# Optimization experiments

Measured on AMD Instinct MI355X. Metric: run time of the kernel, lower is better.

## Reference

```python
import jax, jax.numpy as jnp
import numpy as np

B, T, E, H, DK, FF = 8, 2048, 64, 8, 8, 256
EPS = 1e-5


def _ln(x, g, b):
    m = jnp.mean(x, axis=-1, keepdims=True)
    v = jnp.mean((x - m) ** 2, axis=-1, keepdims=True)
    return (x - m) * jax.lax.rsqrt(v + EPS) * g + b


def setup_inputs() -> dict:
    key = jax.random.key(0)
    ks = jax.random.split(key, 16)
    s = 0.05
    f32 = jnp.float32
    return {
        "x": jax.random.normal(ks[0], (B, T, E), f32),
        "Wq": jax.random.normal(ks[1], (E, E), f32) * s,
        "bq": jnp.zeros((E,), f32),
        "Wk": jax.random.normal(ks[2], (E, E), f32) * s,
        "bk": jnp.zeros((E,), f32),
        "Wv": jax.random.normal(ks[3], (E, E), f32) * s,
        "bv": jnp.zeros((E,), f32),
        "Wo": jax.random.normal(ks[4], (E, E), f32) * s,
        "bo": jnp.zeros((E,), f32),
        "theta_attn": jax.random.uniform(ks[5], (), f32, 0.0, 2.0 * np.pi),
        "theta_ffn": jax.random.uniform(ks[6], (), f32, 0.0, 2.0 * np.pi),
        "W1": jax.random.normal(ks[7], (FF, E), f32) * s,
        "b1": jnp.zeros((FF,), f32),
        "W2": jax.random.normal(ks[8], (E, FF), f32) * s,
        "b2": jnp.zeros((E,), f32),
        "g1": jnp.ones((E,), f32),
        "be1": jnp.zeros((E,), f32),
        "g2": jnp.ones((E,), f32),
        "be2": jnp.zeros((E,), f32),
    }


def _forward(x, Wq, bq, Wk, bk, Wv, bv, Wo, bo, theta_attn, theta_ffn,
             W1, b1, W2, b2, g1, be1, g2, be2):
    def split(h):  # [B,T,E] -> [B,H,T,DK]
        return h.reshape(B, T, H, DK).transpose(0, 2, 1, 3)

    q = split(x @ Wq.T + bq)
    k = split(x @ Wk.T + bk)
    v = split(x @ Wv.T + bv)
    # per-head quantum circuit: RX(x) then shared RX(theta) -> <Z> = cos(x + theta)
    q = jnp.cos(q + theta_attn)
    k = jnp.cos(k + theta_attn)
    v = jnp.cos(v + theta_attn)
    scores = jnp.einsum('bhtd,bhsd->bhts', q, k) / np.float32(np.sqrt(DK))
    scores = jax.nn.softmax(scores, axis=-1)
    attn = jnp.einsum('bhts,bhsd->bhtd', scores, v)
    attn = attn.transpose(0, 2, 1, 3).reshape(B, T, E) @ Wo.T + bo
    x1 = _ln(x + attn, g1, be1)
    # FFN quantum circuit: RX(x) then shared RY(theta) -> <Z> = cos(x)*cos(theta)
    qout = jnp.cos(x1) * jnp.cos(theta_ffn)
    f = jax.nn.relu(qout @ W1.T + b1) @ W2.T + b2
    return _ln(x1 + f, g2, be2)


def reference(x, Wq, bq, Wk, bk, Wv, bv, Wo, bo, theta_attn, theta_ffn,
              W1, b1, W2, b2, g1, be1, g2, be2):
    return _forward(x, Wq, bq, Wk, bk, Wv, bv, Wo, bo, theta_attn, theta_ffn,
                    W1, b1, W2, b2, g1, be1, g2, be2)
```

## Files before the change

### kernel.cpp

```cpp
#include <hip/hip_runtime.h>
#include <hip/hip_bf16.h>

#define B_ 8
#define T_ 2048
#define NROWS 16384

typedef __attribute__((ext_vector_type(16))) float f32x16;
typedef __attribute__((ext_vector_type(8))) short short8;
typedef __fp16 half2_t __attribute__((ext_vector_type(2)));

__device__ __forceinline__ unsigned int pkrtz(float a, float b) {
    half2_t h = __builtin_amdgcn_cvt_pkrtz(a, b);
    return __builtin_bit_cast(unsigned int, h);
}
__device__ __forceinline__ unsigned int pkbf(float a, float b) {
    return __builtin_amdgcn_perm(__float_as_uint(b), __float_as_uint(a), 0x07060302u);
}
__device__ __forceinline__ float dot2(unsigned int a, unsigned int b, float c) {
    return __builtin_amdgcn_fdot2(__builtin_bit_cast(half2_t, a),
                                  __builtin_bit_cast(half2_t, b), c, false);
}
__device__ __forceinline__ float fast_exp2(float x) {
#if __has_builtin(__builtin_amdgcn_exp2f)
    return __builtin_amdgcn_exp2f(x);
#else
    return exp2f(x);
#endif
}

__global__ __launch_bounds__(512, 2) void qkv_kernel(
    const float* __restrict__ x,
    const float* __restrict__ Wq, const float* __restrict__ bq,
    const float* __restrict__ Wk, const float* __restrict__ bk,
    const float* __restrict__ Wv, const float* __restrict__ bv,
    const float* __restrict__ theta_attn,
    unsigned short* __restrict__ qb, unsigned short* __restrict__ kbuf,
    unsigned short* __restrict__ vbuf)
{
    __shared__ unsigned int xpk[32 * 66];
    __shared__ unsigned int wpk[32 * 196];
    __shared__ unsigned int outs[6144];
    const int tid = threadIdx.x;
    const int n0 = blockIdx.x * 64;

    #pragma unroll
    for (int t = 0; t < 2; t++) {
        int fi = tid + t * 512;
        float4 v = ((const float4*)(x + (size_t)n0 * 64))[fi];
        int r = fi >> 4, k0 = (fi & 15) * 4;
        xpk[(k0 >> 1) * 66 + r] = pkrtz(v.x, v.y);
        xpk[((k0 >> 1) + 1) * 66 + r] = pkrtz(v.z, v.w);
    }
    const float* Wm[3] = {Wq, Wk, Wv};
    #pragma unroll
    for (int t = 0; t < 6; t++) {
        int fi = tid + t * 512;
        int m = fi >> 10, j = (fi >> 4) & 63, k0 = (fi & 15) * 4;
        float4 v = ((const float4*)Wm[m])[fi & 1023];
        wpk[(k0 >> 1) * 196 + m * 64 + j] = pkrtz(v.x, v.y);
        wpk[((k0 >> 1) + 1) * 196 + m * 64 + j] = pkrtz(v.z, v.w);
    }
    __syncthreads();

    const int r0 = (tid & 31) * 2;
    const int c0 = (tid >> 5) * 12;
    float acc[2][12] = {};
    #pragma unroll 8
    for (int kp = 0; kp < 32; kp++) {
        uint2 a = *(const uint2*)&xpk[kp * 66 + r0];
        uint4 b0 = *(const uint4*)&wpk[kp * 196 + c0];
        uint4 b1 = *(const uint4*)&wpk[kp * 196 + c0 + 4];
        uint4 b2 = *(const uint4*)&wpk[kp * 196 + c0 + 8];
        unsigned int bb[12] = {b0.x, b0.y, b0.z, b0.w,
                               b1.x, b1.y, b1.z, b1.w,
                               b2.x, b2.y, b2.z, b2.w};
        #pragma unroll
        for (int j = 0; j < 12; j++) {
            acc[0][j] = dot2(a.x, bb[j], acc[0][j]);
            acc[1][j] = dot2(a.y, bb[j], acc[1][j]);
        }
    }

    {
        const float th = *theta_attn;
        const float QS = 0.51006980f;
        const float* biasp[3] = {bq, bk, bv};
        float bcol[12];
        #pragma unroll
        for (int j = 0; j < 12; j++) {
            int c = c0 + j;
            bcol[j] = biasp[c >> 6][c & 63];
        }
        #pragma unroll
        for (int i = 0; i < 2; i++) {
            float vals[12];
            #pragma unroll
            for (int j = 0; j < 12; j++) {
                float v = __cosf(acc[i][j] + bcol[j] + th);
                vals[j] = ((c0 + j) >> 6) == 0 ? v * QS : v;
            }
            int row = r0 + i;
            #pragma unroll
            for (int t = 0; t < 6; t++) {
                int c = c0 + 2 * t;
                outs[(c >> 3) * 256 + row * 4 + ((c & 7) >> 1)] = pkbf(vals[2*t], vals[2*t+1]);
            }
        }
    }
    __syncthreads();

    unsigned short* outp3[3] = {qb, kbuf, vbuf};
    #pragma unroll
    for (int t = 0; t < 3; t++) {
        int fi = tid + t * 512;
        int bh = fi >> 6, r2 = fi & 63;
        int m = bh >> 3, hI = bh & 7;
        uint4 v = *(const uint4*)&outs[4 * fi];
        int n = n0 + r2;
        unsigned short* dst = outp3[m] +
            ((size_t)((n >> 11) * 8 + hI) * 2048 + (n & 2047)) * 8;
        *(uint4*)dst = v;
    }
}

__global__ __launch_bounds__(256, 4) void attn_kernel(
    const unsigned short* __restrict__ qb,
    const unsigned short* __restrict__ kbuf,
    const unsigned short* __restrict__ vbuf,
    float* __restrict__ attn)
{
    __shared__ __align__(16) unsigned short Ks[1024 * 8];
    __shared__ __align__(16) unsigned short Vt[9 * 1032];
    const int tid = threadIdx.x;
    const int head = blockIdx.x >> 4;
    const int qblk = blockIdx.x & 15;
    const size_t hoff = (size_t)head * T_ * 8;
    const int wave = tid >> 6, lane = tid & 63;
    const int col = lane & 31, h = lane >> 5;
    const int q0 = qblk * 128 + wave * 32;

    const short8 z8 = {0, 0, 0, 0, 0, 0, 0, 0};
    short8 bqf = z8;
    if (h == 0) bqf = *(const short8*)(qb + hoff + (size_t)(q0 + col) * 8);

    if (tid < 128)
        ((uint4*)(Vt + 8 * 1032))[tid] =
            make_uint4(0x3f803f80u, 0x3f803f80u, 0x3f803f80u, 0x3f803f80u);

    f32x16 oacc = {0.f,0.f,0.f,0.f,0.f,0.f,0.f,0.f,0.f,0.f,0.f,0.f,0.f,0.f,0.f,0.f};
    const f32x16 z16 = {0.f,0.f,0.f,0.f,0.f,0.f,0.f,0.f,0.f,0.f,0.f,0.f,0.f,0.f,0.f,0.f};
    const unsigned short* vbase = &Vt[(col < 9 ? col : 8) * 1032 + 8 * h];
    short8 ak = z8;

    for (int half = 0; half < 2; half++) {
        __syncthreads();
        {
            const uint4* kg = (const uint4*)(kbuf + hoff + (size_t)half * 1024 * 8);
            const uint4* vg = (const uint4*)(vbuf + hoff + (size_t)half * 1024 * 8);
            #pragma unroll
            for (int it = 0; it < 4; it++) {
                int s = tid + it * 256;
                ((uint4*)Ks)[s] = kg[s];
                union { uint4 u; unsigned short us[8]; } cv;
                cv.u = vg[s];
                int sp = (s & ~12) | ((s & 4) << 1) | ((s & 8) >> 1);
                #pragma unroll
                for (int d = 0; d < 8; d++) Vt[d * 1032 + sp] = cv.us[d];
            }
        }
        __syncthreads();

        for (int s0 = 0; s0 < 1024; s0 += 32) {
            if (h == 0) ak = *(const short8*)&Ks[(s0 + col) * 8];
            f32x16 S = __builtin_amdgcn_mfma_f32_32x32x16_bf16(ak, bqf, z16, 0, 0, 0);
            #pragma unroll
            for (int g = 0; g < 2; g++) {
                const int o = g * 8;
                union { unsigned int u[4]; short8 s; } bp;
                bp.u[0] = pkbf(fast_exp2(S[o+0]), fast_exp2(S[o+1]));
                bp.u[1] = pkbf(fast_exp2(S[o+2]), fast_exp2(S[o+3]));
                bp.u[2] = pkbf(fast_exp2(S[o+4]), fast_exp2(S[o+5]));
                bp.u[3] = pkbf(fast_exp2(S[o+6]), fast_exp2(S[o+7]));
                short8 av = *(const short8*)&vbase[s0 + g * 16];
                oacc = __builtin_amdgcn_mfma_f32_32x32x16_bf16(av, bp.s, oacc, 0, 0, 0);
            }
        }
    }

    float tot = oacc[4];
    tot += __shfl_xor(tot, 32);
    const float inv = 1.0f / tot;
    const int bI = head >> 3, hI = head & 7;
    const int q = q0 + col;
    #pragma unroll
    for (int rr = 0; rr < 4; rr++) {
        int d = 4 * h + rr;
        attn[((size_t)bI * 2048 + q) * 64 + hI * 8 + d] = oacc[rr] * inv;
    }
}

__global__ __launch_bounds__(512, 4) void tail_kernel(
    const float* __restrict__ attn, const float* __restrict__ x,
    const float* __restrict__ Wo, const float* __restrict__ bo,
    const float* __restrict__ g1, const float* __restrict__ be1,
    const float* __restrict__ theta_ffn,
    const float* __restrict__ W1, const float* __restrict__ b1,
    const float* __restrict__ W2, const float* __restrict__ b2,
    const float* __restrict__ g2, const float* __restrict__ be2,
    float* __restrict__ outp)
{
    __shared__ unsigned int Wbuf[10496];
    __shared__ unsigned int qpk[32 * 34];
    __shared__ unsigned int Upk[32 * 132];
    const int tid = threadIdx.x;
    const int lane = tid & 63;
    const int n0 = blockIdx.x * 32;
    unsigned int* const W1p = Wbuf + 2176;
    unsigned int* const W2p = Wbuf;
    unsigned int* const hrow = Upk;

    const int rp = ((tid >> 6) & 3) * 4 + (lane & 3);
    const int r0 = rp * 2;
    const int c0 = ((lane >> 2) & 15) * 4;

    float4 atv = ((const float4*)(attn + (size_t)n0 * 64))[tid];
    float4 wo0 = ((const float4*)Wo)[tid];
    float4 wo1 = ((const float4*)Wo)[tid + 512];
    float4 xv0 = *(const float4*)(x + (size_t)(n0 + r0) * 64 + c0);
    float4 xv1 = *(const float4*)(x + (size_t)(n0 + r0 + 1) * 64 + c0);
    float4 w1r[8];
    #pragma unroll
    for (int t = 0; t < 8; t++) w1r[t] = ((const float4*)W1)[tid + t * 512];

    {
        int r = tid >> 4, k0 = (tid & 15) * 4;
        Upk[(k0 >> 1) * 34 + r] = pkrtz(atv.x, atv.y);
        Upk[((k0 >> 1) + 1) * 34 + r] = pkrtz(atv.z, atv.w);
        Wbuf[(k0 >> 1) * 68 + r] = pkrtz(wo0.x, wo0.y);
        Wbuf[((k0 >> 1) + 1) * 68 + r] = pkrtz(wo0.z, wo0.w);
        int fi = tid + 512;
        int r2 = fi >> 4, k2 = (fi & 15) * 4;
        Wbuf[(k2 >> 1) * 68 + r2] = pkrtz(wo1.x, wo1.y);
        Wbuf[((k2 >> 1) + 1) * 68 + r2] = pkrtz(wo1.z, wo1.w);
    }
    __syncthreads();

    #pragma unroll
    for (int t = 0; t < 8; t++) {
        int fi = tid + t * 512;
        int f = fi >> 4, k0 = (fi & 15) * 4;
        W1p[(k0 >> 1) * 260 + f] = pkrtz(w1r[t].x, w1r[t].y);
        W1p[((k0 >> 1) + 1) * 260 + f] = pkrtz(w1r[t].z, w1r[t].w);
    }

    float x1v[2][4];
    if (tid < 256) {
        float acc1[2][4] = {};
        #pragma unroll 8
        for (int kp = 0; kp < 32; kp++) {
            uint2 a = *(const uint2*)&Upk[kp * 34 + r0];
            uint4 b = *(const uint4*)&Wbuf[kp * 68 + c0];
            unsigned int bb[4] = {b.x, b.y, b.z, b.w};
            #pragma unroll
            for (int j = 0; j < 4; j++) {
                acc1[0][j] = dot2(a.x, bb[j], acc1[0][j]);
                acc1[1][j] = dot2(a.y, bb[j], acc1[1][j]);
            }
        }
        float4 bo4 = *(const float4*)&bo[c0];
        float4 g14 = *(const float4*)&g1[c0];
        float4 be14 = *(const float4*)&be1[c0];
        float gg[4] = {g14.x, g14.y, g14.z, g14.w};
        float eb[4] = {be14.x, be14.y, be14.z, be14.w};
        float bb4[4] = {bo4.x, bo4.y, bo4.z, bo4.w};
        float cth = __cosf(*theta_ffn);
        #pragma unroll
        for (int i = 0; i < 2; i++) {
            float4 xv = i ? xv1 : xv0;
            float vv[4] = {xv.x + acc1[i][0] + bb4[0], xv.y + acc1[i][1] + bb4[1],
                           xv.z + acc1[i][2] + bb4[2], xv.w + acc1[i][3] + bb4[3]};
            float s1 = vv[0] + vv[1] + vv[2] + vv[3];
            float s2 = vv[0]*vv[0] + vv[1]*vv[1] + vv[2]*vv[2] + vv[3]*vv[3];
            #pragma unroll
            for (int m = 4; m <= 32; m <<= 1) {
                s1 += __shfl_xor(s1, m);
                s2 += __shfl_xor(s2, m);
            }
            float mean = s1 * 0.015625f;
            float rstd = rsqrtf(s2 * 0.015625f - mean * mean + 1e-5f);
            float qv[4];
            #pragma unroll
            for (int j = 0; j < 4; j++) {
                x1v[i][j] = (vv[j] - mean) * rstd * gg[j] + eb[j];
                qv[j] = __cosf(x1v[i][j]) * cth;
            }
            qpk[((c0 >> 1) + 0) * 34 + r0 + i] = pkrtz(qv[0], qv[1]);
            qpk[((c0 >> 1) + 1) * 34 + r0 + i] = pkrtz(qv[2], qv[3]);
        }
    }
    __syncthreads();

    float4 w2r[8];
    #pragma unroll
    for (int t = 0; t < 8; t++) w2r[t] = ((const float4*)W2)[tid + t * 512];

    {
        const int r2 = (tid & 15) * 2;
        const int f0 = (tid >> 4) * 8;
        float acc2[2][8] = {};
        #pragma unroll 4
        for (int kp = 0; kp < 32; kp++) {
            uint2 a = *(const uint2*)&qpk[kp * 34 + r2];
            uint4 b0 = *(const uint4*)&W1p[kp * 260 + f0];
            uint4 b1q = *(const uint4*)&W1p[kp * 260 + f0 + 4];
            unsigned int bb[8] = {b0.x, b0.y, b0.z, b0.w, b1q.x, b1q.y, b1q.z, b1q.w};
            #pragma unroll
            for (int j = 0; j < 8; j++) {
                acc2[0][j] = dot2(a.x, bb[j], acc2[0][j]);
                acc2[1][j] = dot2(a.y, bb[j], acc2[1][j]);
            }
        }
        float4 c1a = *(const float4*)&b1[f0];
        float4 c1b = *(const float4*)&b1[f0 + 4];
        float bb[8] = {c1a.x, c1a.y, c1a.z, c1a.w, c1b.x, c1b.y, c1b.z, c1b.w};
        __syncthreads();
        #pragma unroll
        for (int i = 0; i < 2; i++) {
            float hv[8];
            #pragma unroll
            for (int j = 0; j < 8; j++) hv[j] = fmaxf(acc2[i][j] + bb[j], 0.f);
            uint4 hq;
            hq.x = pkrtz(hv[0], hv[1]); hq.y = pkrtz(hv[2], hv[3]);
            hq.z = pkrtz(hv[4], hv[5]); hq.w = pkrtz(hv[6], hv[7]);
            *(uint4*)&hrow[(r2 + i) * 132 + (f0 >> 1)] = hq;
        }
    }

    #pragma unroll
    for (int t = 0; t < 8; t++) {
        int fi = tid + t * 512;
        int e = fi >> 6, k0 = (fi & 63) * 4;
        W2p[(k0 >> 1) * 68 + e] = pkrtz(w2r[t].x, w2r[t].y);
        W2p[((k0 >> 1) + 1) * 68 + e] = pkrtz(w2r[t].z, w2r[t].w);
    }
    __syncthreads();

    if (tid < 256) {
        float acc3[2][4] = {};
        #pragma unroll 4
        for (int fp0 = 0; fp0 < 128; fp0 += 4) {
            uint4 a0 = *(const uint4*)&hrow[(r0 + 0) * 132 + fp0];
            uint4 a1 = *(const uint4*)&hrow[(r0 + 1) * 132 + fp0];
            uint4 b0 = *(const uint4*)&W2p[(fp0 + 0) * 68 + c0];
            uint4 b1q = *(const uint4*)&W2p[(fp0 + 1) * 68 + c0];
            uint4 b2q = *(const uint4*)&W2p[(fp0 + 2) * 68 + c0];
            uint4 b3q = *(const uint4*)&W2p[(fp0 + 3) * 68 + c0];
            unsigned int aa[2][4] = {{a0.x, a0.y, a0.z, a0.w},
                                     {a1.x, a1.y, a1.z, a1.w}};
            unsigned int bbb[4][4] = {{b0.x, b0.y, b0.z, b0.w},
                                      {b1q.x, b1q.y, b1q.z, b1q.w},
                                      {b2q.x, b2q.y, b2q.z, b2q.w},
                                      {b3q.x, b3q.y, b3q.z, b3q.w}};
            #pragma unroll
            for (int i = 0; i < 2; i++)
                #pragma unroll
                for (int j = 0; j < 4; j++) {
                    float t0 = dot2(aa[i][0], bbb[0][j], acc3[i][j]);
                    t0 = dot2(aa[i][1], bbb[1][j], t0);
                    t0 = dot2(aa[i][2], bbb[2][j], t0);
                    acc3[i][j] = dot2(aa[i][3], bbb[3][j], t0);
                }
        }
        float4 b24 = *(const float4*)&b2[c0];
        float4 g24 = *(const float4*)&g2[c0];
        float4 be24 = *(const float4*)&be2[c0];
        #pragma unroll
        for (int i = 0; i < 2; i++) {
            float vv[4] = {x1v[i][0] + acc3[i][0] + b24.x,
                           x1v[i][1] + acc3[i][1] + b24.y,
                           x1v[i][2] + acc3[i][2] + b24.z,
                           x1v[i][3] + acc3[i][3] + b24.w};
            float s1 = vv[0] + vv[1] + vv[2] + vv[3];
            float s2 = vv[0]*vv[0] + vv[1]*vv[1] + vv[2]*vv[2] + vv[3]*vv[3];
            #pragma unroll
            for (int m = 4; m <= 32; m <<= 1) {
                s1 += __shfl_xor(s1, m);
                s2 += __shfl_xor(s2, m);
            }
            float mean = s1 * 0.015625f;
            float rstd = rsqrtf(s2 * 0.015625f - mean * mean + 1e-5f);
            float4 o;
            o.x = (vv[0] - mean) * rstd * g24.x + be24.x;
            o.y = (vv[1] - mean) * rstd * g24.y + be24.y;
            o.z = (vv[2] - mean) * rstd * g24.z + be24.z;
            o.w = (vv[3] - mean) * rstd * g24.w + be24.w;
            *(float4*)(outp + (size_t)(n0 + r0 + i) * 64 + c0) = o;
        }
    }
}

extern "C" void kernel_launch(void* const* d_in, const int* in_sizes, int n_in,
                              void* d_out, int out_size, void* d_ws, size_t ws_size,
                              hipStream_t stream)
{
    const float* x   = (const float*)d_in[0];
    const float* Wq  = (const float*)d_in[1];
    const float* bq  = (const float*)d_in[2];
    const float* Wk  = (const float*)d_in[3];
    const float* bk  = (const float*)d_in[4];
    const float* Wv  = (const float*)d_in[5];
    const float* bv  = (const float*)d_in[6];
    const float* Wo  = (const float*)d_in[7];
    const float* bo  = (const float*)d_in[8];
    const float* tha = (const float*)d_in[9];
    const float* thf = (const float*)d_in[10];
    const float* W1  = (const float*)d_in[11];
    const float* b1  = (const float*)d_in[12];
    const float* W2  = (const float*)d_in[13];
    const float* b2  = (const float*)d_in[14];
    const float* g1  = (const float*)d_in[15];
    const float* be1 = (const float*)d_in[16];
    const float* g2  = (const float*)d_in[17];
    const float* be2 = (const float*)d_in[18];

    char* wsb = (char*)d_ws;
    unsigned short* qbp = (unsigned short*)(wsb);
    unsigned short* kbp = (unsigned short*)(wsb + (2u << 20));
    unsigned short* vbp = (unsigned short*)(wsb + (4u << 20));
    float* attn = (float*)(wsb + (6u << 20));

    qkv_kernel<<<256, 512, 0, stream>>>(x, Wq, bq, Wk, bk, Wv, bv, tha, qbp, kbp, vbp);
    attn_kernel<<<1024, 256, 0, stream>>>(qbp, kbp, vbp, attn);
    tail_kernel<<<512, 512, 0, stream>>>(attn, x, Wo, bo, g1, be1, thf,
                                         W1, b1, W2, b2, g2, be2, (float*)d_out);
}
```

Measured before the change: 148.7 us.

## Use MFMA 32x32x16 f16 for tail kernel's three GEMMs

Replaces the fdot2-based scalar-ish matmuls in the tail kernel (Wo projection, W1 FFN, W2 FFN) with 32x32x16 f16 MFMA instructions. Shared-memory layouts are changed to row-major K-contiguous packed halves, and results are staged through LDS so every thread handles one row-slice for the layernorms. This aims to cut VALU work in the tail, at the cost of extra syncs and LDS staging, with only two waves active for the 64-wide GEMMs.

```diff
diff --git a/kernel.cpp b/kernel.cpp
--- a/kernel.cpp
+++ b/kernel.cpp
@@ -8,6 +8,7 @@
 typedef __attribute__((ext_vector_type(16))) float f32x16;
 typedef __attribute__((ext_vector_type(8))) short short8;
 typedef __fp16 half2_t __attribute__((ext_vector_type(2)));
+typedef __fp16 half8_t __attribute__((ext_vector_type(8)));
 
 __device__ __forceinline__ unsigned int pkrtz(float a, float b) {
     half2_t h = __builtin_amdgcn_cvt_pkrtz(a, b);
@@ -209,39 +210,45 @@
     const float* __restrict__ g2, const float* __restrict__ be2,
     float* __restrict__ outp)
 {
-    __shared__ unsigned int Wbuf[10496];
-    __shared__ unsigned int qpk[32 * 34];
-    __shared__ unsigned int Upk[32 * 132];
+    __shared__ unsigned int smem[15744];
     const int tid = threadIdx.x;
     const int lane = tid & 63;
+    const int wave = tid >> 6;
+    const int h = lane >> 5;
     const int n0 = blockIdx.x * 32;
-    unsigned int* const W1p = Wbuf + 2176;
-    unsigned int* const W2p = Wbuf;
-    unsigned int* const hrow = Upk;
-
-    const int rp = ((tid >> 6) & 3) * 4 + (lane & 3);
-    const int r0 = rp * 2;
-    const int c0 = ((lane >> 2) & 15) * 4;
+    const int mrow = tid >> 4;
+    const int c0 = (tid & 15) * 4;
+
+    unsigned int* const W1p = smem;
+    unsigned int* const W2p = smem;
+    unsigned int* const Atp = smem + 9216;
+    unsigned int* const qoutp = smem + 9216;
+    unsigned int* const Wop = smem + 10368;
+    unsigned int* const hrowp = smem + 10368;
+    float* const Yf = (float*)(smem + 12672);
+    float* const Y2a = (float*)(smem + 14592);
+    float* const Y2b = (float*)(smem + 8448);
+
+    const f32x16 z16 = {0.f,0.f,0.f,0.f,0.f,0.f,0.f,0.f,0.f,0.f,0.f,0.f,0.f,0.f,0.f,0.f};
 
     float4 atv = ((const float4*)(attn + (size_t)n0 * 64))[tid];
     float4 wo0 = ((const float4*)Wo)[tid];
     float4 wo1 = ((const float4*)Wo)[tid + 512];
-    float4 xv0 = *(const float4*)(x + (size_t)(n0 + r0) * 64 + c0);
-    float4 xv1 = *(const float4*)(x + (size_t)(n0 + r0 + 1) * 64 + c0);
+    float4 xv = *(const float4*)(x + (size_t)(n0 + mrow) * 64 + c0);
     float4 w1r[8];
     #pragma unroll
     for (int t = 0; t < 8; t++) w1r[t] = ((const float4*)W1)[tid + t * 512];
 
     {
         int r = tid >> 4, k0 = (tid & 15) * 4;
-        Upk[(k0 >> 1) * 34 + r] = pkrtz(atv.x, atv.y);
-        Upk[((k0 >> 1) + 1) * 34 + r] = pkrtz(atv.z, atv.w);
-        Wbuf[(k0 >> 1) * 68 + r] = pkrtz(wo0.x, wo0.y);
-        Wbuf[((k0 >> 1) + 1) * 68 + r] = pkrtz(wo0.z, wo0.w);
+        uint2 a2 = make_uint2(pkrtz(atv.x, atv.y), pkrtz(atv.z, atv.w));
+        *(uint2*)&Atp[r * 36 + (k0 >> 1)] = a2;
+        uint2 wa = make_uint2(pkrtz(wo0.x, wo0.y), pkrtz(wo0.z, wo0.w));
+        *(uint2*)&Wop[r * 36 + (k0 >> 1)] = wa;
         int fi = tid + 512;
-        int r2 = fi >> 4, k2 = (fi & 15) * 4;
-        Wbuf[(k2 >> 1) * 68 + r2] = pkrtz(wo1.x, wo1.y);
-        Wbuf[((k2 >> 1) + 1) * 68 + r2] = pkrtz(wo1.z, wo1.w);
+        int e1 = fi >> 4, k1 = (fi & 15) * 4;
+        uint2 wb = make_uint2(pkrtz(wo1.x, wo1.y), pkrtz(wo1.z, wo1.w));
+        *(uint2*)&Wop[e1 * 36 + (k1 >> 1)] = wb;
     }
     __syncthreads();
 
@@ -249,54 +256,56 @@
     for (int t = 0; t < 8; t++) {
         int fi = tid + t * 512;
         int f = fi >> 4, k0 = (fi & 15) * 4;
-        W1p[(k0 >> 1) * 260 + f] = pkrtz(w1r[t].x, w1r[t].y);
-        W1p[((k0 >> 1) + 1) * 260 + f] = pkrtz(w1r[t].z, w1r[t].w);
-    }
-
-    float x1v[2][4];
-    if (tid < 256) {
-        float acc1[2][4] = {};
-        #pragma unroll 8
-        for (int kp = 0; kp < 32; kp++) {
-            uint2 a = *(const uint2*)&Upk[kp * 34 + r0];
-            uint4 b = *(const uint4*)&Wbuf[kp * 68 + c0];
-            unsigned int bb[4] = {b.x, b.y, b.z, b.w};
-            #pragma unroll
-            for (int j = 0; j < 4; j++) {
-                acc1[0][j] = dot2(a.x, bb[j], acc1[0][j]);
-                acc1[1][j] = dot2(a.y, bb[j], acc1[1][j]);
-            }
-        }
-        float4 bo4 = *(const float4*)&bo[c0];
+        uint2 w2 = make_uint2(pkrtz(w1r[t].x, w1r[t].y), pkrtz(w1r[t].z, w1r[t].w));
+        *(uint2*)&W1p[f * 36 + (k0 >> 1)] = w2;
+    }
+
+    if (wave < 2) {
+        const int colo = wave * 32 + (lane & 31);
+        f32x16 acc = z16;
+        #pragma unroll
+        for (int kk = 0; kk < 4; kk++) {
+            half8_t a = __builtin_bit_cast(half8_t,
+                *(const uint4*)&Atp[(lane & 31) * 36 + kk * 8 + h * 4]);
+            half8_t b = __builtin_bit_cast(half8_t,
+                *(const uint4*)&Wop[colo * 36 + kk * 8 + h * 4]);
+            acc = __builtin_amdgcn_mfma_f32_32x32x16_f16(a, b, acc, 0, 0, 0);
+        }
+        float bov = bo[colo];
+        #pragma unroll
+        for (int reg = 0; reg < 16; reg++) {
+            int rr = (reg & 3) + 8 * (reg >> 2) + 4 * h;
+            Yf[rr * 68 + colo] = acc[reg] + bov;
+        }
+    }
+    __syncthreads();
+
+    float x1v[4];
+    {
+        float4 yv = *(const float4*)&Yf[mrow * 68 + c0];
+        float vv[4] = {xv.x + yv.x, xv.y + yv.y, xv.z + yv.z, xv.w + yv.w};
+        float s1 = vv[0] + vv[1] + vv[2] + vv[3];
+        float s2 = vv[0]*vv[0] + vv[1]*vv[1] + vv[2]*vv[2] + vv[3]*vv[3];
+        #pragma unroll
+        for (int m = 1; m <= 8; m <<= 1) {
+            s1 += __shfl_xor(s1, m);
+            s2 += __shfl_xor(s2, m);
+        }
+        float mean = s1 * 0.015625f;
+        float rstd = rsqrtf(s2 * 0.015625f - mean * mean + 1e-5f);
         float4 g14 = *(const float4*)&g1[c0];
         float4 be14 = *(const float4*)&be1[c0];
         float gg[4] = {g14.x, g14.y, g14.z, g14.w};
         float eb[4] = {be14.x, be14.y, be14.z, be14.w};
-        float bb4[4] = {bo4.x, bo4.y, bo4.z, bo4.w};
         float cth = __cosf(*theta_ffn);
-        #pragma unroll
-        for (int i = 0; i < 2; i++) {
-            float4 xv = i ? xv1 : xv0;
-            float vv[4] = {xv.x + acc1[i][0] + bb4[0], xv.y + acc1[i][1] + bb4[1],
-                           xv.z + acc1[i][2] + bb4[2], xv.w + acc1[i][3] + bb4[3]};
-            float s1 = vv[0] + vv[1] + vv[2] + vv[3];
-            float s2 = vv[0]*vv[0] + vv[1]*vv[1] + vv[2]*vv[2] + vv[3]*vv[3];
-            #pragma unroll
-            for (int m = 4; m <= 32; m <<= 1) {
-                s1 += __shfl_xor(s1, m);
-                s2 += __shfl_xor(s2, m);
-            }
-            float mean = s1 * 0.015625f;
-            float rstd = rsqrtf(s2 * 0.015625f - mean * mean + 1e-5f);
-            float qv[4];
-            #pragma unroll
-            for (int j = 0; j < 4; j++) {
-                x1v[i][j] = (vv[j] - mean) * rstd * gg[j] + eb[j];
-                qv[j] = __cosf(x1v[i][j]) * cth;
-            }
-            qpk[((c0 >> 1) + 0) * 34 + r0 + i] = pkrtz(qv[0], qv[1]);
-            qpk[((c0 >> 1) + 1) * 34 + r0 + i] = pkrtz(qv[2], qv[3]);
-        }
+        float qv[4];
+        #pragma unroll
+        for (int j = 0; j < 4; j++) {
+            x1v[j] = (vv[j] - mean) * rstd * gg[j] + eb[j];
+            qv[j] = __cosf(x1v[j]) * cth;
+        }
+        uint2 q2 = make_uint2(pkrtz(qv[0], qv[1]), pkrtz(qv[2], qv[3]));
+        *(uint2*)&qoutp[mrow * 36 + (c0 >> 1)] = q2;
     }
     __syncthreads();
 
@@ -305,97 +314,83 @@
     for (int t = 0; t < 8; t++) w2r[t] = ((const float4*)W2)[tid + t * 512];
 
     {
-        const int r2 = (tid & 15) * 2;
-        const int f0 = (tid >> 4) * 8;
-        float acc2[2][8] = {};
-        #pragma unroll 4
-        for (int kp = 0; kp < 32; kp++) {
-            uint2 a = *(const uint2*)&qpk[kp * 34 + r2];
-            uint4 b0 = *(const uint4*)&W1p[kp * 260 + f0];
-            uint4 b1q = *(const uint4*)&W1p[kp * 260 + f0 + 4];
-            unsigned int bb[8] = {b0.x, b0.y, b0.z, b0.w, b1q.x, b1q.y, b1q.z, b1q.w};
-            #pragma unroll
-            for (int j = 0; j < 8; j++) {
-                acc2[0][j] = dot2(a.x, bb[j], acc2[0][j]);
-                acc2[1][j] = dot2(a.y, bb[j], acc2[1][j]);
-            }
-        }
-        float4 c1a = *(const float4*)&b1[f0];
-        float4 c1b = *(const float4*)&b1[f0 + 4];
-        float bb[8] = {c1a.x, c1a.y, c1a.z, c1a.w, c1b.x, c1b.y, c1b.z, c1b.w};
-        __syncthreads();
-        #pragma unroll
-        for (int i = 0; i < 2; i++) {
-            float hv[8];
-            #pragma unroll
-            for (int j = 0; j < 8; j++) hv[j] = fmaxf(acc2[i][j] + bb[j], 0.f);
-            uint4 hq;
-            hq.x = pkrtz(hv[0], hv[1]); hq.y = pkrtz(hv[2], hv[3]);
-            hq.z = pkrtz(hv[4], hv[5]); hq.w = pkrtz(hv[6], hv[7]);
-            *(uint4*)&hrow[(r2 + i) * 132 + (f0 >> 1)] = hq;
-        }
-    }
+        const int fl = lane & 31;
+        f32x16 acc = z16;
+        #pragma unroll
+        for (int kk = 0; kk < 4; kk++) {
+            half8_t a = __builtin_bit_cast(half8_t,
+                *(const uint4*)&W1p[(wave * 32 + fl) * 36 + kk * 8 + h * 4]);
+            half8_t b = __builtin_bit_cast(half8_t,
+                *(const uint4*)&qoutp[fl * 36 + kk * 8 + h * 4]);
+            acc = __builtin_amdgcn_mfma_f32_32x32x16_f16(a, b, acc, 0, 0, 0);
+        }
+        const int row = lane & 31;
+        #pragma unroll
+        for (int q = 0; q < 4; q++) {
+            int fb = wave * 32 + 8 * q + 4 * h;
+            float4 b1v = *(const float4*)&b1[fb];
+            float h0 = fmaxf(acc[4*q+0] + b1v.x, 0.f);
+            float h1 = fmaxf(acc[4*q+1] + b1v.y, 0.f);
+            float h2 = fmaxf(acc[4*q+2] + b1v.z, 0.f);
+            float h3 = fmaxf(acc[4*q+3] + b1v.w, 0.f);
+            uint2 hp = make_uint2(pkrtz(h0, h1), pkrtz(h2, h3));
+            *(uint2*)&hrowp[row * 132 + (fb >> 1)] = hp;
+        }
+    }
+    __syncthreads();
 
     #pragma unroll
     for (int t = 0; t < 8; t++) {
         int fi = tid + t * 512;
         int e = fi >> 6, k0 = (fi & 63) * 4;
-        W2p[(k0 >> 1) * 68 + e] = pkrtz(w2r[t].x, w2r[t].y);
-        W2p[((k0 >> 1) + 1) * 68 + e] = pkrtz(w2r[t].z, w2r[t].w);
-    }
-    __syncthreads();
-
-    if (tid < 256) {
-        float acc3[2][4] = {};
-        #pragma unroll 4
-        for (int fp0 = 0; fp0 < 128; fp0 += 4) {
-            uint4 a0 = *(const uint4*)&hrow[(r0 + 0) * 132 + fp0];
-            uint4 a1 = *(const uint4*)&hrow[(r0 + 1) * 132 + fp0];
-            uint4 b0 = *(const uint4*)&W2p[(fp0 + 0) * 68 + c0];
-            uint4 b1q = *(const uint4*)&W2p[(fp0 + 1) * 68 + c0];
-            uint4 b2q = *(const uint4*)&W2p[(fp0 + 2) * 68 + c0];
-            uint4 b3q = *(const uint4*)&W2p[(fp0 + 3) * 68 + c0];
-            unsigned int aa[2][4] = {{a0.x, a0.y, a0.z, a0.w},
-                                     {a1.x, a1.y, a1.z, a1.w}};
-            unsigned int bbb[4][4] = {{b0.x, b0.y, b0.z, b0.w},
-                                      {b1q.x, b1q.y, b1q.z, b1q.w},
-                                      {b2q.x, b2q.y, b2q.z, b2q.w},
-                                      {b3q.x, b3q.y, b3q.z, b3q.w}};
-            #pragma unroll
-            for (int i = 0; i < 2; i++)
-                #pragma unroll
-                for (int j = 0; j < 4; j++) {
-                    float t0 = dot2(aa[i][0], bbb[0][j], acc3[i][j]);
-                    t0 = dot2(aa[i][1], bbb[1][j], t0);
-                    t0 = dot2(aa[i][2], bbb[2][j], t0);
-                    acc3[i][j] = dot2(aa[i][3], bbb[3][j], t0);
-                }
-        }
-        float4 b24 = *(const float4*)&b2[c0];
+        uint2 w2 = make_uint2(pkrtz(w2r[t].x, w2r[t].y), pkrtz(w2r[t].z, w2r[t].w));
+        *(uint2*)&W2p[e * 132 + (k0 >> 1)] = w2;
+    }
+    __syncthreads();
+
+    if (wave < 2) {
+        const int colo = wave * 32 + (lane & 31);
+        f32x16 acc = z16;
+        #pragma unroll
+        for (int kk = 0; kk < 16; kk++) {
+            half8_t a = __builtin_bit_cast(half8_t,
+                *(const uint4*)&hrowp[(lane & 31) * 132 + kk * 8 + h * 4]);
+            half8_t b = __builtin_bit_cast(half8_t,
+                *(const uint4*)&W2p[colo * 132 + kk * 8 + h * 4]);
+            acc = __builtin_amdgcn_mfma_f32_32x32x16_f16(a, b, acc, 0, 0, 0);
+        }
+        float b2v = b2[colo];
+        float* Ydst = wave ? Y2b : Y2a;
+        const int cl = lane & 31;
+        #pragma unroll
+        for (int reg = 0; reg < 16; reg++) {
+            int rr = (reg & 3) + 8 * (reg >> 2) + 4 * h;
+            Ydst[rr * 36 + cl] = acc[reg] + b2v;
+        }
+    }
+    __syncthreads();
+
+    {
+        float4 fv = (c0 < 32) ? *(const float4*)&Y2a[mrow * 36 + c0]
+                              : *(const float4*)&Y2b[mrow * 36 + (c0 - 32)];
+        float vv[4] = {x1v[0] + fv.x, x1v[1] + fv.y, x1v[2] + fv.z, x1v[3] + fv.w};
+        float s1 = vv[0] + vv[1] + vv[2] + vv[3];
+        float s2 = vv[0]*vv[0] + vv[1]*vv[1] + vv[2]*vv[2] + vv[3]*vv[3];
+        #pragma unroll
+        for (int m = 1; m <= 8; m <<= 1) {
+            s1 += __shfl_xor(s1, m);
+            s2 += __shfl_xor(s2, m);
+        }
+        float mean = s1 * 0.015625f;
+        float rstd = rsqrtf(s2 * 0.015625f - mean * mean + 1e-5f);
         float4 g24 = *(const float4*)&g2[c0];
         float4 be24 = *(const float4*)&be2[c0];
-        #pragma unroll
-        for (int i = 0; i < 2; i++) {
-            float vv[4] = {x1v[i][0] + acc3[i][0] + b24.x,
-                           x1v[i][1] + acc3[i][1] + b24.y,
-                           x1v[i][2] + acc3[i][2] + b24.z,
-                           x1v[i][3] + acc3[i][3] + b24.w};
-            float s1 = vv[0] + vv[1] + vv[2] + vv[3];
-            float s2 = vv[0]*vv[0] + vv[1]*vv[1] + vv[2]*vv[2] + vv[3]*vv[3];
-            #pragma unroll
-            for (int m = 4; m <= 32; m <<= 1) {
-                s1 += __shfl_xor(s1, m);
-                s2 += __shfl_xor(s2, m);
-            }
-            float mean = s1 * 0.015625f;
-            float rstd = rsqrtf(s2 * 0.015625f - mean * mean + 1e-5f);
-            float4 o;
-            o.x = (vv[0] - mean) * rstd * g24.x + be24.x;
-            o.y = (vv[1] - mean) * rstd * g24.y + be24.y;
-            o.z = (vv[2] - mean) * rstd * g24.z + be24.z;
-            o.w = (vv[3] - mean) * rstd * g24.w + be24.w;
-            *(float4*)(outp + (size_t)(n0 + r0 + i) * 64 + c0) = o;
-        }
+        float4 o;
+        o.x = (vv[0] - mean) * rstd * g24.x + be24.x;
+        o.y = (vv[1] - mean) * rstd * g24.y + be24.y;
+        o.z = (vv[2] - mean) * rstd * g24.z + be24.z;
+        o.w = (vv[3] - mean) * rstd * g24.w + be24.w;
+        *(float4*)(outp + (size_t)(n0 + mrow) * 64 + c0) = o;
     }
 }
 
```

After: 136.8 us. 8.0% less time.
